# Optimization experiments

Measured on AMD Instinct MI355X. Metric: run time of the kernel, lower is better.

## Reference

```python
import jax, jax.numpy as jnp
import numpy as np

B, L, D = 1, 512, 1024
NH, NKV, NR = 16, 4, 16
HD, RD = 64, 64
NREP = NH // NKV  # 4
ATTN_SCALE = 1.0 / float(np.sqrt(HD))
REL_SCALE = 1.0 / float(np.sqrt(RD))


def setup_inputs() -> dict:
    key = jax.random.key(0)
    ks = jax.random.split(key, 9)
    x = jax.random.normal(ks[0], (B, L, D), jnp.float32)
    symbols = jax.random.normal(ks[1], (B, L, D), jnp.float32)
    # standard llama-style RoPE frequencies: [L, HD//2]
    inv_freq = 1.0 / (10000.0 ** (np.arange(0, HD, 2, dtype=np.float32) / HD))
    f = np.outer(np.arange(L, dtype=np.float32), inv_freq)
    freqs_cos = jnp.asarray(np.cos(f), jnp.float32)
    freqs_sin = jnp.asarray(np.sin(f), jnp.float32)
    s = 0.02
    wq_attn = jax.random.normal(ks[2], (D, NH * HD), jnp.float32) * s
    wk_attn = jax.random.normal(ks[3], (D, NKV * HD), jnp.float32) * s
    wq_rel = jax.random.normal(ks[4], (D, NR * RD), jnp.float32) * s
    wk_rel = jax.random.normal(ks[5], (D, NR * RD), jnp.float32) * s
    wr = jax.random.normal(ks[6], (NR, NH * HD), jnp.float32) * s
    wv = jax.random.normal(ks[7], (D, NKV * HD), jnp.float32) * s
    wo = jax.random.normal(ks[8], (NH * HD, NH * HD), jnp.float32) * s
    return dict(x=x, symbols=symbols, freqs_cos=freqs_cos, freqs_sin=freqs_sin,
                wq_attn=wq_attn, wk_attn=wk_attn, wq_rel=wq_rel, wk_rel=wk_rel,
                wr=wr, wv=wv, wo=wo)


def _rope(t, cos, sin):
    # t: [b, l, h, hd]; cos/sin: [l, hd//2]
    tr = t.reshape(t.shape[:-1] + (HD // 2, 2))
    re, im = tr[..., 0], tr[..., 1]
    c = cos[None, :, None, :]
    s = sin[None, :, None, :]
    out = jnp.stack([re * c - im * s, re * s + im * c], axis=-1)
    return out.reshape(t.shape)


def reference(x, symbols, freqs_cos, freqs_sin, wq_attn, wk_attn, wq_rel, wk_rel, wr, wv, wo):
    b, l, _ = x.shape
    q = (x @ wq_attn).reshape(b, l, NH, HD)
    k = (x @ wk_attn).reshape(b, l, NKV, HD)
    qr = (x @ wq_rel).reshape(b, l, NR, RD)
    kr = (x @ wk_rel).reshape(b, l, NR, RD)
    sv = (symbols @ wv).reshape(b, l, NKV, HD)
    q = _rope(q, freqs_cos, freqs_sin)
    k = _rope(k, freqs_cos, freqs_sin)
    # GQA: repeat kv heads consecutively (matches torch repeat_kv expand+reshape)
    k = jnp.repeat(k, NREP, axis=2)
    sv = jnp.repeat(sv, NREP, axis=2)
    scores = jnp.einsum('bihd,bjhd->bhij', q, k) * ATTN_SCALE
    causal = jnp.tril(jnp.ones((l, l), bool))
    scores = jnp.where(causal[None, None], scores, -jnp.inf)
    attn = jax.nn.softmax(scores, axis=-1)  # [b, nh, l, l]
    # relation scores, identity activation, laid out as [b, i, j, nr]
    relations = jnp.einsum('bird,bjrd->bijr', qr, kr) * REL_SCALE
    proj_rel = (relations @ wr).reshape(b, l, l, NH, HD)  # dominant intermediate
    attended_symbols = jnp.einsum('bhij,bjhd->bihd', attn, sv)
    attended_relations = jnp.einsum('bhij,bijhd->bihd', attn, proj_rel)
    out = (attended_symbols + attended_relations).reshape(b, l, NH * HD) @ wo
    return out, attn, relations
```

## Files before the change

### kernel.cpp

```cpp
#include <hip/hip_runtime.h>
#include <math.h>

#define ATTN_SCALE 0.125f
#define REL_SCALE 0.125f

using ushort = unsigned short;
using bf16x8 = __attribute__((ext_vector_type(8))) __bf16;
using floatx4 = __attribute__((ext_vector_type(4))) float;
using ushort8 = __attribute__((ext_vector_type(8))) ushort;
using ushort4v = __attribute__((ext_vector_type(4))) ushort;

__device__ __forceinline__ ushort f2bf(float x) {
  unsigned int u = __builtin_bit_cast(unsigned int, x);
  u += 0x7fffu + ((u >> 16) & 1u);
  return (ushort)(u >> 16);
}
__device__ __forceinline__ float bf2f(ushort h) {
  return __builtin_bit_cast(float, (unsigned int)h << 16);
}

template <bool AF32>
__device__ __forceinline__ void mfma_body(const void* __restrict__ Av, int lda,
                                          const ushort* __restrict__ Bt, int ldb,
                                          int K, floatx4 (&acc)[2][2]) {
  __shared__ ushort As[64][72];
  __shared__ ushort Bs[64][72];
  const int tid = threadIdx.x;
  const int sr = tid >> 2, sc = (tid & 3) << 4;
  const int lane = tid & 63;
  const int wy = (tid >> 7) & 1, wx = (tid >> 6) & 1;
  const int lm = lane & 15, lq = lane >> 4;
  const ushort* a_rd = &As[32 * wy + lm][lq * 8];
  const ushort* b_rd = &Bs[32 * wx + lm][lq * 8];
  for (int k0 = 0; k0 < K; k0 += 64) {
    ushort8 av0, av1;
    if constexpr (AF32) {
      const float* Ap = (const float*)Av + (size_t)sr * lda + k0 + sc;
      float4 f0 = *(const float4*)(Ap);
      float4 f1 = *(const float4*)(Ap + 4);
      float4 f2 = *(const float4*)(Ap + 8);
      float4 f3 = *(const float4*)(Ap + 12);
      av0 = ushort8{f2bf(f0.x), f2bf(f0.y), f2bf(f0.z), f2bf(f0.w),
                    f2bf(f1.x), f2bf(f1.y), f2bf(f1.z), f2bf(f1.w)};
      av1 = ushort8{f2bf(f2.x), f2bf(f2.y), f2bf(f2.z), f2bf(f2.w),
                    f2bf(f3.x), f2bf(f3.y), f2bf(f3.z), f2bf(f3.w)};
    } else {
      const ushort* Ap = (const ushort*)Av + (size_t)sr * lda + k0 + sc;
      av0 = *(const ushort8*)Ap;
      av1 = *(const ushort8*)(Ap + 8);
    }
    const ushort* Bp = Bt + (size_t)sr * ldb + k0 + sc;
    ushort8 bv0 = *(const ushort8*)Bp;
    ushort8 bv1 = *(const ushort8*)(Bp + 8);
    __syncthreads();
    *(ushort8*)&As[sr][sc] = av0;
    *(ushort8*)&As[sr][sc + 8] = av1;
    *(ushort8*)&Bs[sr][sc] = bv0;
    *(ushort8*)&Bs[sr][sc + 8] = bv1;
    __syncthreads();
#pragma unroll
    for (int kh = 0; kh < 2; ++kh) {
      bf16x8 a0 = *(const bf16x8*)(a_rd + kh * 32);
      bf16x8 a1 = *(const bf16x8*)(a_rd + 16 * 72 + kh * 32);
      bf16x8 b0 = *(const bf16x8*)(b_rd + kh * 32);
      bf16x8 b1 = *(const bf16x8*)(b_rd + 16 * 72 + kh * 32);
      acc[0][0] = __builtin_amdgcn_mfma_f32_16x16x32_bf16(a0, b0, acc[0][0], 0, 0, 0);
      acc[0][1] = __builtin_amdgcn_mfma_f32_16x16x32_bf16(a0, b1, acc[0][1], 0, 0, 0);
      acc[1][0] = __builtin_amdgcn_mfma_f32_16x16x32_bf16(a1, b0, acc[1][0], 0, 0, 0);
      acc[1][1] = __builtin_amdgcn_mfma_f32_16x16x32_bf16(a1, b1, acc[1][1], 0, 0, 0);
    }
  }
}

#define EPILOG_VARS                                                   \
  const int lane = threadIdx.x & 63;                                  \
  const int wy = (threadIdx.x >> 7) & 1, wx = (threadIdx.x >> 6) & 1; \
  const int lm = lane & 15, lq = lane >> 4;

__global__ __launch_bounds__(256) void prep_kernel(
    const float* __restrict__ x, const float* __restrict__ sym,
    const float* __restrict__ wq, const float* __restrict__ wk,
    const float* __restrict__ wqr, const float* __restrict__ wkr,
    const float* __restrict__ wv, const float* __restrict__ wo,
    ushort* __restrict__ xb, ushort* __restrict__ symb,
    ushort* __restrict__ wqT, ushort* __restrict__ wkT, ushort* __restrict__ wqrT,
    ushort* __restrict__ wkrT, ushort* __restrict__ wvT, ushort* __restrict__ woT) {
  if (blockIdx.z == 6) {
    int b = blockIdx.y * 32 + blockIdx.x;
    if (b >= 512) return;
    int idx = b * 256 + threadIdx.x;
    int i4 = idx << 2;
    float4 v = *(const float4*)(x + i4);
    uint2 o;
    o.x = (unsigned)f2bf(v.x) | ((unsigned)f2bf(v.y) << 16);
    o.y = (unsigned)f2bf(v.z) | ((unsigned)f2bf(v.w) << 16);
    *(uint2*)(xb + i4) = o;
    float4 w = *(const float4*)(sym + i4);
    o.x = (unsigned)f2bf(w.x) | ((unsigned)f2bf(w.y) << 16);
    o.y = (unsigned)f2bf(w.z) | ((unsigned)f2bf(w.w) << 16);
    *(uint2*)(symb + i4) = o;
    return;
  }
  __shared__ ushort t[32][33];
  const float* in;
  ushort* out;
  int N;
  switch (blockIdx.z) {
    case 0: in = wq;  out = wqT;  N = 1024; break;
    case 1: in = wk;  out = wkT;  N = 256;  break;
    case 2: in = wqr; out = wqrT; N = 1024; break;
    case 3: in = wkr; out = wkrT; N = 1024; break;
    case 4: in = wv;  out = wvT;  N = 256;  break;
    default: in = wo; out = woT;  N = 1024; break;
  }
  int n0 = blockIdx.x << 5;
  if (n0 >= N) return;
  int k0 = blockIdx.y << 5;
  int tx = threadIdx.x & 31, ty = threadIdx.x >> 5;
#pragma unroll
  for (int rr = 0; rr < 32; rr += 8)
    t[ty + rr][tx] = f2bf(in[(size_t)(k0 + ty + rr) * N + n0 + tx]);
  __syncthreads();
#pragma unroll
  for (int rr = 0; rr < 32; rr += 8)
    out[(size_t)(n0 + ty + rr) * 1024 + k0 + tx] = t[tx][ty + rr];
}

__global__ __launch_bounds__(256) void proj_mfma(
    const ushort* __restrict__ xb, const ushort* __restrict__ symb,
    const ushort* __restrict__ wqT, const ushort* __restrict__ wkT,
    const ushort* __restrict__ wqrT, const ushort* __restrict__ wkrT,
    const ushort* __restrict__ wvT,
    ushort* __restrict__ qb, ushort* __restrict__ kb, ushort* __restrict__ qrb,
    ushort* __restrict__ krb, ushort* __restrict__ svT,
    const float* __restrict__ fcos, const float* __restrict__ fsin) {
  const int z = blockIdx.z;
  const ushort* A = xb;
  const ushort* Bt;
  ushort* C;
  int N;
  switch (z) {
    case 0: Bt = wqT;  C = qb;  N = 1024; break;
    case 1: Bt = wkT;  C = kb;  N = 256;  break;
    case 2: Bt = wqrT; C = qrb; N = 1024; break;
    case 3: Bt = wkrT; C = krb; N = 1024; break;
    default: A = symb; Bt = wvT; C = svT; N = 256; break;
  }
  const int bn = blockIdx.x << 6;
  if (bn >= N) return;
  const int bm = blockIdx.y << 6;
  floatx4 acc[2][2] = {};
  mfma_body<false>(A + (size_t)bm * 1024, 1024, Bt + (size_t)bn * 1024, 1024, 1024, acc);
  EPILOG_VARS
  if (z <= 1) {
#pragma unroll
    for (int sy = 0; sy < 2; ++sy)
#pragma unroll
      for (int sx = 0; sx < 2; ++sx)
#pragma unroll
        for (int e = 0; e < 4; ++e) {
          int row = bm + 32 * wy + 16 * sy + 4 * lq + e;
          int col = bn + 32 * wx + 16 * sx + lm;
          float v = acc[sy][sx][e];
          float pv = __shfl_xor(v, 1);
          int d = col & 63, p = d >> 1;
          float c = fcos[(row << 5) + p], s = fsin[(row << 5) + p];
          float o = (d & 1) ? fmaf(pv, s, v * c) : fmaf(v, c, -pv * s);
          C[(size_t)row * N + col] = f2bf(o);
        }
  } else if (z == 4) {
#pragma unroll
    for (int sy = 0; sy < 2; ++sy)
#pragma unroll
      for (int sx = 0; sx < 2; ++sx)
#pragma unroll
        for (int e = 0; e < 4; ++e) {
          int row = bm + 32 * wy + 16 * sy + 4 * lq + e;
          int col = bn + 32 * wx + 16 * sx + lm;
          svT[(size_t)col * 512 + row] = f2bf(acc[sy][sx][e]);
        }
  } else {
#pragma unroll
    for (int sy = 0; sy < 2; ++sy)
#pragma unroll
      for (int sx = 0; sx < 2; ++sx)
#pragma unroll
        for (int e = 0; e < 4; ++e) {
          int row = bm + 32 * wy + 16 * sy + 4 * lq + e;
          int col = bn + 32 * wx + 16 * sx + lm;
          C[(size_t)row * N + col] = f2bf(acc[sy][sx][e]);
        }
  }
}

__global__ __launch_bounds__(256) void relations_mfma(const ushort* __restrict__ qrb,
                                                      const ushort* __restrict__ krb,
                                                      float* __restrict__ rel) {
  const int bi0 = blockIdx.y << 5, bj0 = blockIdx.x << 5;
  const int tid = threadIdx.x, wave = tid >> 6, lane = tid & 63;
  const int lm = lane & 15, lq = lane >> 4;
  const int ib = bi0 + ((wave >> 1) << 4), jb = bj0 + ((wave & 1) << 4);
  const ushort* qrow = qrb + (size_t)(ib + lm) * 1024 + lq * 8;
  const ushort* krow = krb + (size_t)(jb + lm) * 1024 + lq * 8;
#pragma unroll
  for (int rq = 0; rq < 4; ++rq) {
    floatx4 acc[4];
#pragma unroll
    for (int rr = 0; rr < 4; ++rr) {
      int roff = ((rq << 2) + rr) << 6;
      bf16x8 a0 = *(const bf16x8*)(qrow + roff);
      bf16x8 a1 = *(const bf16x8*)(qrow + roff + 32);
      bf16x8 b0 = *(const bf16x8*)(krow + roff);
      bf16x8 b1 = *(const bf16x8*)(krow + roff + 32);
      floatx4 t = {0.f, 0.f, 0.f, 0.f};
      t = __builtin_amdgcn_mfma_f32_16x16x32_bf16(a0, b0, t, 0, 0, 0);
      t = __builtin_amdgcn_mfma_f32_16x16x32_bf16(a1, b1, t, 0, 0, 0);
      acc[rr] = t;
    }
#pragma unroll
    for (int e = 0; e < 4; ++e) {
      int i = ib + 4 * lq + e, j = jb + lm;
      float4 v = make_float4(acc[0][e] * REL_SCALE, acc[1][e] * REL_SCALE,
                             acc[2][e] * REL_SCALE, acc[3][e] * REL_SCALE);
      *(float4*)(rel + ((size_t)i * 512 + j) * 16 + (rq << 2)) = v;
    }
  }
}

__global__ __launch_bounds__(256) void flash_kernel(const ushort* __restrict__ qb,
                                                    const ushort* __restrict__ kb,
                                                    const ushort* __restrict__ svT,
                                                    float* __restrict__ attn,
                                                    float* __restrict__ asym) {
  __shared__ float S[16][516];
  __shared__ ushort P[16][520];
  const int h = blockIdx.y, i0 = blockIdx.x << 4, kv = h >> 2;
  const int tid = threadIdx.x, wave = tid >> 6, lane = tid & 63;
  const int lm = lane & 15, lq = lane >> 4;
  const int ntiles = blockIdx.x + 1;
  const ushort* qrow = qb + (size_t)(i0 + lm) * 1024 + (h << 6) + lq * 8;
  bf16x8 a0 = *(const bf16x8*)(qrow);
  bf16x8 a1 = *(const bf16x8*)(qrow + 32);
  for (int jt = wave; jt < ntiles; jt += 4) {
    int jb = jt << 4;
    const ushort* krow = kb + (size_t)(jb + lm) * 256 + (kv << 6) + lq * 8;
    bf16x8 b0 = *(const bf16x8*)(krow);
    bf16x8 b1 = *(const bf16x8*)(krow + 32);
    floatx4 acc = {0.f, 0.f, 0.f, 0.f};
    acc = __builtin_amdgcn_mfma_f32_16x16x32_bf16(a0, b0, acc, 0, 0, 0);
    acc = __builtin_amdgcn_mfma_f32_16x16x32_bf16(a1, b1, acc, 0, 0, 0);
#pragma unroll
    for (int e = 0; e < 4; ++e) S[4 * lq + e][jb + lm] = acc[e] * ATTN_SCALE;
  }
  __syncthreads();
  const int row = tid >> 4, t16 = tid & 15;
  const int i = i0 + row;
  const int nj = ntiles << 4;
  float m = -INFINITY;
  for (int s = 0; (s << 6) < nj; ++s) {
    int j4 = (t16 << 2) + (s << 6);
    float4 v = *(const float4*)&S[row][j4];
    if (j4 + 0 <= i) m = fmaxf(m, v.x);
    if (j4 + 1 <= i) m = fmaxf(m, v.y);
    if (j4 + 2 <= i) m = fmaxf(m, v.z);
    if (j4 + 3 <= i) m = fmaxf(m, v.w);
  }
#pragma unroll
  for (int o = 8; o; o >>= 1) m = fmaxf(m, __shfl_xor(m, o, 16));
  float sum = 0.f;
  for (int s = 0; (s << 6) < nj; ++s) {
    int j4 = (t16 << 2) + (s << 6);
    float4 v = *(const float4*)&S[row][j4];
    if (j4 + 0 <= i) sum += __expf(v.x - m);
    if (j4 + 1 <= i) sum += __expf(v.y - m);
    if (j4 + 2 <= i) sum += __expf(v.z - m);
    if (j4 + 3 <= i) sum += __expf(v.w - m);
  }
#pragma unroll
  for (int o = 8; o; o >>= 1) sum += __shfl_xor(sum, o, 16);
  const float inv = 1.f / sum;
  float* arow = attn + (size_t)h * 262144 + (size_t)i * 512;
  for (int s = 0; s < 8; ++s) {
    int j4 = (t16 << 2) + (s << 6);
    float4 o4 = {0.f, 0.f, 0.f, 0.f};
    if (j4 < nj) {
      float4 v = *(const float4*)&S[row][j4];
      o4.x = (j4 + 0 <= i) ? __expf(v.x - m) * inv : 0.f;
      o4.y = (j4 + 1 <= i) ? __expf(v.y - m) * inv : 0.f;
      o4.z = (j4 + 2 <= i) ? __expf(v.z - m) * inv : 0.f;
      o4.w = (j4 + 3 <= i) ? __expf(v.w - m) * inv : 0.f;
    }
    *(float4*)(arow + j4) = o4;
    ushort4v p4;
    p4.x = f2bf(o4.x); p4.y = f2bf(o4.y); p4.z = f2bf(o4.z); p4.w = f2bf(o4.w);
    *(ushort4v*)&P[row][j4] = p4;
  }
  __syncthreads();
  const int dbase = wave << 4;
  floatx4 acc2 = {0.f, 0.f, 0.f, 0.f};
  const ushort* svrow = svT + (size_t)((kv << 6) + dbase + lm) * 512;
  const int kmax = (nj + 31) & ~31;
  for (int kt = 0; kt < kmax; kt += 32) {
    bf16x8 pa = *(const bf16x8*)&P[lm][kt + lq * 8];
    bf16x8 pb = *(const bf16x8*)(svrow + kt + lq * 8);
    acc2 = __builtin_amdgcn_mfma_f32_16x16x32_bf16(pa, pb, acc2, 0, 0, 0);
  }
#pragma unroll
  for (int e = 0; e < 4; ++e)
    asym[(size_t)(i0 + 4 * lq + e) * 1024 + (h << 6) + dbase + lm] = acc2[e];
}

__global__ __launch_bounds__(256) void tker_combine(const float* __restrict__ attn,
                                                    const float* __restrict__ rel,
                                                    const float* __restrict__ asym,
                                                    const float* __restrict__ wr,
                                                    float* __restrict__ att) {
  const int i = blockIdx.x, tid = threadIdx.x;
  __shared__ float a_s[16][132];
  __shared__ float r_s[128][16];
  __shared__ float Ts[16][17];
  const int h = tid >> 4, r = tid & 15;
  float acc = 0.f;
  for (int j0 = 0; j0 <= i; j0 += 128) {
#pragma unroll
    for (int idx = tid; idx < 512; idx += 256) {
      int hh = idx >> 5, j4 = (idx & 31) << 2;
      *(float4*)&a_s[hh][j4] =
          *(const float4*)(attn + (size_t)hh * 262144 + (size_t)i * 512 + j0 + j4);
    }
#pragma unroll
    for (int idx = tid; idx < 512; idx += 256)
      *(float4*)(&r_s[0][0] + (idx << 2)) =
          *(const float4*)(rel + (size_t)i * 8192 + ((size_t)j0 << 4) + (idx << 2));
    __syncthreads();
#pragma unroll 8
    for (int jj = 0; jj < 128; ++jj)
      acc = fmaf(a_s[h][jj], r_s[jj][r], acc);
    __syncthreads();
  }
  Ts[h][r] = acc;
  __syncthreads();
  const int hc = tid >> 4, d4 = (tid & 15) << 2;
  float4 o = *(const float4*)(asym + (size_t)i * 1024 + (hc << 6) + d4);
#pragma unroll
  for (int rr = 0; rr < 16; ++rr) {
    float tv = Ts[hc][rr];
    float4 w4 = *(const float4*)(wr + (size_t)rr * 1024 + (hc << 6) + d4);
    o.x = fmaf(tv, w4.x, o.x);
    o.y = fmaf(tv, w4.y, o.y);
    o.z = fmaf(tv, w4.z, o.z);
    o.w = fmaf(tv, w4.w, o.w);
  }
  *(float4*)(att + (size_t)i * 1024 + (hc << 6) + d4) = o;
}

__global__ __launch_bounds__(256) void out_mfma(const float* __restrict__ att,
                                                const ushort* __restrict__ woT,
                                                float* __restrict__ out) {
  const int bn = blockIdx.x << 6, bm = blockIdx.y << 6;
  floatx4 acc[2][2] = {};
  mfma_body<true>(att + (size_t)bm * 1024, 1024, woT + (size_t)bn * 1024, 1024, 1024, acc);
  EPILOG_VARS
#pragma unroll
  for (int sy = 0; sy < 2; ++sy)
#pragma unroll
    for (int sx = 0; sx < 2; ++sx)
#pragma unroll
      for (int e = 0; e < 4; ++e) {
        int row = bm + 32 * wy + 16 * sy + 4 * lq + e;
        int col = bn + 32 * wx + 16 * sx + lm;
        out[(size_t)row * 1024 + col] = acc[sy][sx][e];
      }
}

extern "C" void kernel_launch(void* const* d_in, const int* in_sizes, int n_in,
                              void* d_out, int out_size, void* d_ws, size_t ws_size,
                              hipStream_t stream) {
  const float* x       = (const float*)d_in[0];
  const float* symbols = (const float*)d_in[1];
  const float* fcos    = (const float*)d_in[2];
  const float* fsin    = (const float*)d_in[3];
  const float* wq_attn = (const float*)d_in[4];
  const float* wk_attn = (const float*)d_in[5];
  const float* wq_rel  = (const float*)d_in[6];
  const float* wk_rel  = (const float*)d_in[7];
  const float* wr      = (const float*)d_in[8];
  const float* wv      = (const float*)d_in[9];
  const float* wo      = (const float*)d_in[10];

  float* out  = (float*)d_out;
  float* attn = out + 524288;
  float* rel  = attn + 4194304;

  char* wsb = (char*)d_ws;
  const size_t MB = 1 << 20;
  ushort* xb   = (ushort*)(wsb);
  ushort* symb = (ushort*)(wsb + 1 * MB);
  ushort* wqT  = (ushort*)(wsb + 2 * MB);
  ushort* wkT  = (ushort*)(wsb + 4 * MB);
  ushort* wqrT = (ushort*)(wsb + 4 * MB + 512 * 1024);
  ushort* wkrT = (ushort*)(wsb + 6 * MB + 512 * 1024);
  ushort* wvT  = (ushort*)(wsb + 8 * MB + 512 * 1024);
  ushort* woT  = (ushort*)(wsb + 9 * MB);
  ushort* qb   = (ushort*)(wsb + 11 * MB);
  ushort* kb   = (ushort*)(wsb + 12 * MB);
  ushort* qrb  = (ushort*)(wsb + 12 * MB + 256 * 1024);
  ushort* krb  = (ushort*)(wsb + 13 * MB + 256 * 1024);
  ushort* svT  = (ushort*)(wsb + 14 * MB + 256 * 1024);
  float*  asym = (float*)(wsb + 2 * MB);
  float*  att  = (float*)(wsb + 4 * MB + 512 * 1024);

  prep_kernel<<<dim3(32, 32, 7), 256, 0, stream>>>(x, symbols, wq_attn, wk_attn,
                                                   wq_rel, wk_rel, wv, wo,
                                                   xb, symb, wqT, wkT, wqrT, wkrT, wvT, woT);
  proj_mfma<<<dim3(16, 8, 5), 256, 0, stream>>>(xb, symb, wqT, wkT, wqrT, wkrT, wvT,
                                                qb, kb, qrb, krb, svT, fcos, fsin);
  relations_mfma<<<dim3(16, 16), 256, 0, stream>>>(qrb, krb, rel);
  flash_kernel<<<dim3(32, 16), 256, 0, stream>>>(qb, kb, svT, attn, asym);
  tker_combine<<<dim3(512), 256, 0, stream>>>(attn, rel, asym, wr, att);
  out_mfma<<<dim3(16, 8), 256, 0, stream>>>(att, woT, out);
}
```

Before: 169.3 us.

## Merge relations and flash kernels, bf16 attention output, smaller out GEMM tiles

Fuses the relations GEMM and the causal flash-attention kernel into one launch of 768 blocks. The first 512 blocks run attention, scheduled with the heaviest query tiles first, and the rest compute relations, so the two overlap and the causal load is balanced. The combine kernel now stores relations transposed in shared memory so it can use vectorized float4 reads, and writes its output as bf16 rather than fp32. The output GEMM consumes that bf16 input directly and uses 64x32 tiles for twice as many blocks. The trade-offs are an extra transposed scatter into shared memory and bf16 rounding of the combined activations.

```diff
diff --git a/kernel.cpp b/kernel.cpp
--- a/kernel.cpp
+++ b/kernel.cpp
@@ -15,12 +15,8 @@
   u += 0x7fffu + ((u >> 16) & 1u);
   return (ushort)(u >> 16);
 }
-__device__ __forceinline__ float bf2f(ushort h) {
-  return __builtin_bit_cast(float, (unsigned int)h << 16);
-}
-
-template <bool AF32>
-__device__ __forceinline__ void mfma_body(const void* __restrict__ Av, int lda,
+
+__device__ __forceinline__ void mfma_body(const ushort* __restrict__ A, int lda,
                                           const ushort* __restrict__ Bt, int ldb,
                                           int K, floatx4 (&acc)[2][2]) {
   __shared__ ushort As[64][72];
@@ -33,22 +29,9 @@
   const ushort* a_rd = &As[32 * wy + lm][lq * 8];
   const ushort* b_rd = &Bs[32 * wx + lm][lq * 8];
   for (int k0 = 0; k0 < K; k0 += 64) {
-    ushort8 av0, av1;
-    if constexpr (AF32) {
-      const float* Ap = (const float*)Av + (size_t)sr * lda + k0 + sc;
-      float4 f0 = *(const float4*)(Ap);
-      float4 f1 = *(const float4*)(Ap + 4);
-      float4 f2 = *(const float4*)(Ap + 8);
-      float4 f3 = *(const float4*)(Ap + 12);
-      av0 = ushort8{f2bf(f0.x), f2bf(f0.y), f2bf(f0.z), f2bf(f0.w),
-                    f2bf(f1.x), f2bf(f1.y), f2bf(f1.z), f2bf(f1.w)};
-      av1 = ushort8{f2bf(f2.x), f2bf(f2.y), f2bf(f2.z), f2bf(f2.w),
-                    f2bf(f3.x), f2bf(f3.y), f2bf(f3.z), f2bf(f3.w)};
-    } else {
-      const ushort* Ap = (const ushort*)Av + (size_t)sr * lda + k0 + sc;
-      av0 = *(const ushort8*)Ap;
-      av1 = *(const ushort8*)(Ap + 8);
-    }
+    const ushort* Ap = A + (size_t)sr * lda + k0 + sc;
+    ushort8 av0 = *(const ushort8*)Ap;
+    ushort8 av1 = *(const ushort8*)(Ap + 8);
     const ushort* Bp = Bt + (size_t)sr * ldb + k0 + sc;
     ushort8 bv0 = *(const ushort8*)Bp;
     ushort8 bv1 = *(const ushort8*)(Bp + 8);
@@ -150,7 +133,7 @@
   if (bn >= N) return;
   const int bm = blockIdx.y << 6;
   floatx4 acc[2][2] = {};
-  mfma_body<false>(A + (size_t)bm * 1024, 1024, Bt + (size_t)bn * 1024, 1024, 1024, acc);
+  mfma_body(A + (size_t)bm * 1024, 1024, Bt + (size_t)bn * 1024, 1024, 1024, acc);
   EPILOG_VARS
   if (z <= 1) {
 #pragma unroll
@@ -193,51 +176,50 @@
   }
 }
 
-__global__ __launch_bounds__(256) void relations_mfma(const ushort* __restrict__ qrb,
-                                                      const ushort* __restrict__ krb,
-                                                      float* __restrict__ rel) {
-  const int bi0 = blockIdx.y << 5, bj0 = blockIdx.x << 5;
+__global__ __launch_bounds__(256) void relflash_kernel(
+    const ushort* __restrict__ qb, const ushort* __restrict__ kb,
+    const ushort* __restrict__ svT, const ushort* __restrict__ qrb,
+    const ushort* __restrict__ krb, float* __restrict__ attn,
+    float* __restrict__ asym, float* __restrict__ rel) {
+  __shared__ float S[16][516];
+  __shared__ ushort P[16][520];
+  const int bx = blockIdx.x;
   const int tid = threadIdx.x, wave = tid >> 6, lane = tid & 63;
   const int lm = lane & 15, lq = lane >> 4;
-  const int ib = bi0 + ((wave >> 1) << 4), jb = bj0 + ((wave & 1) << 4);
-  const ushort* qrow = qrb + (size_t)(ib + lm) * 1024 + lq * 8;
-  const ushort* krow = krb + (size_t)(jb + lm) * 1024 + lq * 8;
-#pragma unroll
-  for (int rq = 0; rq < 4; ++rq) {
-    floatx4 acc[4];
-#pragma unroll
-    for (int rr = 0; rr < 4; ++rr) {
-      int roff = ((rq << 2) + rr) << 6;
-      bf16x8 a0 = *(const bf16x8*)(qrow + roff);
-      bf16x8 a1 = *(const bf16x8*)(qrow + roff + 32);
-      bf16x8 b0 = *(const bf16x8*)(krow + roff);
-      bf16x8 b1 = *(const bf16x8*)(krow + roff + 32);
-      floatx4 t = {0.f, 0.f, 0.f, 0.f};
-      t = __builtin_amdgcn_mfma_f32_16x16x32_bf16(a0, b0, t, 0, 0, 0);
-      t = __builtin_amdgcn_mfma_f32_16x16x32_bf16(a1, b1, t, 0, 0, 0);
-      acc[rr] = t;
-    }
-#pragma unroll
-    for (int e = 0; e < 4; ++e) {
-      int i = ib + 4 * lq + e, j = jb + lm;
-      float4 v = make_float4(acc[0][e] * REL_SCALE, acc[1][e] * REL_SCALE,
-                             acc[2][e] * REL_SCALE, acc[3][e] * REL_SCALE);
-      *(float4*)(rel + ((size_t)i * 512 + j) * 16 + (rq << 2)) = v;
-    }
-  }
-}
-
-__global__ __launch_bounds__(256) void flash_kernel(const ushort* __restrict__ qb,
-                                                    const ushort* __restrict__ kb,
-                                                    const ushort* __restrict__ svT,
-                                                    float* __restrict__ attn,
-                                                    float* __restrict__ asym) {
-  __shared__ float S[16][516];
-  __shared__ ushort P[16][520];
-  const int h = blockIdx.y, i0 = blockIdx.x << 4, kv = h >> 2;
-  const int tid = threadIdx.x, wave = tid >> 6, lane = tid & 63;
-  const int lm = lane & 15, lq = lane >> 4;
-  const int ntiles = blockIdx.x + 1;
+  if (bx >= 512) {
+    const int b = bx - 512;
+    const int bi0 = (b >> 4) << 5, bj0 = (b & 15) << 5;
+    const int ib = bi0 + ((wave >> 1) << 4), jb = bj0 + ((wave & 1) << 4);
+    const ushort* qrow = qrb + (size_t)(ib + lm) * 1024 + lq * 8;
+    const ushort* krow = krb + (size_t)(jb + lm) * 1024 + lq * 8;
+#pragma unroll
+    for (int rq = 0; rq < 4; ++rq) {
+      floatx4 acc[4];
+#pragma unroll
+      for (int rr = 0; rr < 4; ++rr) {
+        int roff = ((rq << 2) + rr) << 6;
+        bf16x8 a0 = *(const bf16x8*)(qrow + roff);
+        bf16x8 a1 = *(const bf16x8*)(qrow + roff + 32);
+        bf16x8 b0 = *(const bf16x8*)(krow + roff);
+        bf16x8 b1 = *(const bf16x8*)(krow + roff + 32);
+        floatx4 t = {0.f, 0.f, 0.f, 0.f};
+        t = __builtin_amdgcn_mfma_f32_16x16x32_bf16(a0, b0, t, 0, 0, 0);
+        t = __builtin_amdgcn_mfma_f32_16x16x32_bf16(a1, b1, t, 0, 0, 0);
+        acc[rr] = t;
+      }
+#pragma unroll
+      for (int e = 0; e < 4; ++e) {
+        int i = ib + 4 * lq + e, j = jb + lm;
+        float4 v = make_float4(acc[0][e] * REL_SCALE, acc[1][e] * REL_SCALE,
+                               acc[2][e] * REL_SCALE, acc[3][e] * REL_SCALE);
+        *(float4*)(rel + ((size_t)i * 512 + j) * 16 + (rq << 2)) = v;
+      }
+    }
+    return;
+  }
+  const int h = bx >> 5, it = 31 - (bx & 31);
+  const int i0 = it << 4, kv = h >> 2;
+  const int ntiles = it + 1;
   const ushort* qrow = qb + (size_t)(i0 + lm) * 1024 + (h << 6) + lq * 8;
   bf16x8 a0 = *(const bf16x8*)(qrow);
   bf16x8 a1 = *(const bf16x8*)(qrow + 32);
@@ -314,10 +296,10 @@
                                                     const float* __restrict__ rel,
                                                     const float* __restrict__ asym,
                                                     const float* __restrict__ wr,
-                                                    float* __restrict__ att) {
+                                                    ushort* __restrict__ attb) {
   const int i = blockIdx.x, tid = threadIdx.x;
   __shared__ float a_s[16][132];
-  __shared__ float r_s[128][16];
+  __shared__ float r_s[16][132];
   __shared__ float Ts[16][17];
   const int h = tid >> 4, r = tid & 15;
   float acc = 0.f;
@@ -329,13 +311,24 @@
           *(const float4*)(attn + (size_t)hh * 262144 + (size_t)i * 512 + j0 + j4);
     }
 #pragma unroll
-    for (int idx = tid; idx < 512; idx += 256)
-      *(float4*)(&r_s[0][0] + (idx << 2)) =
-          *(const float4*)(rel + (size_t)i * 8192 + ((size_t)j0 << 4) + (idx << 2));
-    __syncthreads();
-#pragma unroll 8
-    for (int jj = 0; jj < 128; ++jj)
-      acc = fmaf(a_s[h][jj], r_s[jj][r], acc);
+    for (int idx = tid; idx < 512; idx += 256) {
+      int j = idx >> 2, r4 = (idx & 3) << 2;
+      float4 v = *(const float4*)(rel + ((size_t)i * 512 + j0 + j) * 16 + r4);
+      r_s[r4 + 0][j] = v.x;
+      r_s[r4 + 1][j] = v.y;
+      r_s[r4 + 2][j] = v.z;
+      r_s[r4 + 3][j] = v.w;
+    }
+    __syncthreads();
+#pragma unroll
+    for (int jj = 0; jj < 128; jj += 4) {
+      float4 a4 = *(const float4*)&a_s[h][jj];
+      float4 r4v = *(const float4*)&r_s[r][jj];
+      acc = fmaf(a4.x, r4v.x, acc);
+      acc = fmaf(a4.y, r4v.y, acc);
+      acc = fmaf(a4.z, r4v.z, acc);
+      acc = fmaf(a4.w, r4v.w, acc);
+    }
     __syncthreads();
   }
   Ts[h][r] = acc;
@@ -351,26 +344,53 @@
     o.z = fmaf(tv, w4.z, o.z);
     o.w = fmaf(tv, w4.w, o.w);
   }
-  *(float4*)(att + (size_t)i * 1024 + (hc << 6) + d4) = o;
-}
-
-__global__ __launch_bounds__(256) void out_mfma(const float* __restrict__ att,
+  ushort4v ob;
+  ob.x = f2bf(o.x); ob.y = f2bf(o.y); ob.z = f2bf(o.z); ob.w = f2bf(o.w);
+  *(ushort4v*)(attb + (size_t)i * 1024 + (hc << 6) + d4) = ob;
+}
+
+__global__ __launch_bounds__(256) void out_mfma(const ushort* __restrict__ attb,
                                                 const ushort* __restrict__ woT,
                                                 float* __restrict__ out) {
-  const int bn = blockIdx.x << 6, bm = blockIdx.y << 6;
-  floatx4 acc[2][2] = {};
-  mfma_body<true>(att + (size_t)bm * 1024, 1024, woT + (size_t)bn * 1024, 1024, 1024, acc);
-  EPILOG_VARS
+  __shared__ ushort As[64][72];
+  __shared__ ushort Bs[32][72];
+  const int bn = blockIdx.x << 5, bm = blockIdx.y << 6;
+  const int tid = threadIdx.x;
+  const int sr = tid >> 2, sc = (tid & 3) << 4;
+  const int br = tid >> 3, bc = (tid & 7) << 3;
+  const int lane = tid & 63;
+  const int wy = (tid >> 7) & 1, wx = (tid >> 6) & 1;
+  const int lm = lane & 15, lq = lane >> 4;
+  const ushort* a_rd = &As[32 * wy + lm][lq * 8];
+  const ushort* b_rd = &Bs[16 * wx + lm][lq * 8];
+  floatx4 acc[2] = {};
+  for (int k0 = 0; k0 < 1024; k0 += 64) {
+    const ushort* Ap = attb + (size_t)(bm + sr) * 1024 + k0 + sc;
+    ushort8 av0 = *(const ushort8*)Ap;
+    ushort8 av1 = *(const ushort8*)(Ap + 8);
+    ushort8 bv = *(const ushort8*)(woT + (size_t)(bn + br) * 1024 + k0 + bc);
+    __syncthreads();
+    *(ushort8*)&As[sr][sc] = av0;
+    *(ushort8*)&As[sr][sc + 8] = av1;
+    *(ushort8*)&Bs[br][bc] = bv;
+    __syncthreads();
+#pragma unroll
+    for (int kh = 0; kh < 2; ++kh) {
+      bf16x8 a0 = *(const bf16x8*)(a_rd + kh * 32);
+      bf16x8 a1 = *(const bf16x8*)(a_rd + 16 * 72 + kh * 32);
+      bf16x8 b0 = *(const bf16x8*)(b_rd + kh * 32);
+      acc[0] = __builtin_amdgcn_mfma_f32_16x16x32_bf16(a0, b0, acc[0], 0, 0, 0);
+      acc[1] = __builtin_amdgcn_mfma_f32_16x16x32_bf16(a1, b0, acc[1], 0, 0, 0);
+    }
+  }
 #pragma unroll
   for (int sy = 0; sy < 2; ++sy)
 #pragma unroll
-    for (int sx = 0; sx < 2; ++sx)
-#pragma unroll
-      for (int e = 0; e < 4; ++e) {
-        int row = bm + 32 * wy + 16 * sy + 4 * lq + e;
-        int col = bn + 32 * wx + 16 * sx + lm;
-        out[(size_t)row * 1024 + col] = acc[sy][sx][e];
-      }
+    for (int e = 0; e < 4; ++e) {
+      int row = bm + 32 * wy + 16 * sy + 4 * lq + e;
+      int col = bn + 16 * wx + lm;
+      out[(size_t)row * 1024 + col] = acc[sy][e];
+    }
 }
 
 extern "C" void kernel_launch(void* const* d_in, const int* in_sizes, int n_in,
@@ -408,15 +428,14 @@
   ushort* krb  = (ushort*)(wsb + 13 * MB + 256 * 1024);
   ushort* svT  = (ushort*)(wsb + 14 * MB + 256 * 1024);
   float*  asym = (float*)(wsb + 2 * MB);
-  float*  att  = (float*)(wsb + 4 * MB + 512 * 1024);
+  ushort* attb = (ushort*)(wsb + 4 * MB + 512 * 1024);
 
   prep_kernel<<<dim3(32, 32, 7), 256, 0, stream>>>(x, symbols, wq_attn, wk_attn,
                                                    wq_rel, wk_rel, wv, wo,
                                                    xb, symb, wqT, wkT, wqrT, wkrT, wvT, woT);
   proj_mfma<<<dim3(16, 8, 5), 256, 0, stream>>>(xb, symb, wqT, wkT, wqrT, wkrT, wvT,
                                                 qb, kb, qrb, krb, svT, fcos, fsin);
-  relations_mfma<<<dim3(16, 16), 256, 0, stream>>>(qrb, krb, rel);
-  flash_kernel<<<dim3(32, 16), 256, 0, stream>>>(qb, kb, svT, attn, asym);
-  tker_combine<<<dim3(512), 256, 0, stream>>>(attn, rel, asym, wr, att);
-  out_mfma<<<dim3(16, 8), 256, 0, stream>>>(att, woT, out);
-}
+  relflash_kernel<<<dim3(768), 256, 0, stream>>>(qb, kb, svT, qrb, krb, attn, asym, rel);
+  tker_combine<<<dim3(512), 256, 0, stream>>>(attn, rel, asym, wr, attb);
+  out_mfma<<<dim3(32, 8), 256, 0, stream>>>(attb, woT, out);
+}
```

Result: faster. 153.8 us (-9.2%).
